# Kernel tuning notes

Hardware: AMD Instinct MI355X
Metric: run time of the kernel (lower is better)

## Reference

```python
import jax, jax.numpy as jnp
import numpy as np

N_NODES = 50000
NUM_FEATS = 512
HIDDEN = 128
NUM_LAYERS = 4
NUM_CLASSES = 40
N_EDGES = 800000
ALPHA = 0.1
C_MIN = 0.2
RESIDUAL_WEIGHT = C_MIN - ALPHA  # 0.1
BIAS_SRELU = -10.0


def setup_inputs() -> dict:
    key = jax.random.key(0)
    ks = jax.random.split(key, 8)
    x = jax.random.normal(ks[0], (N_NODES, NUM_FEATS), dtype=jnp.float32)
    edge_index = jax.random.randint(ks[1], (2, N_EDGES), 0, N_NODES, dtype=jnp.int64)
    W_in = jax.random.normal(ks[2], (NUM_FEATS, HIDDEN), dtype=jnp.float32) / np.sqrt(NUM_FEATS)
    b_in = jnp.zeros((HIDDEN,), dtype=jnp.float32)
    W_layers = jax.random.normal(ks[3], (NUM_LAYERS, HIDDEN, HIDDEN), dtype=jnp.float32) / np.sqrt(HIDDEN)
    srelu_bias = jnp.full((NUM_LAYERS, HIDDEN), BIAS_SRELU, dtype=jnp.float32)
    W_out = jax.random.normal(ks[4], (HIDDEN, NUM_CLASSES), dtype=jnp.float32) / np.sqrt(HIDDEN)
    b_out = jnp.zeros((NUM_CLASSES,), dtype=jnp.float32)
    return {"x": x, "edge_index": edge_index, "W_in": W_in, "b_in": b_in,
            "W_layers": W_layers, "srelu_bias": srelu_bias,
            "W_out": W_out, "b_out": b_out}


def _gcn_norm(edge_index, n):
    # PyG gcn_norm: add self-loops, symmetric normalization D^-1/2 A D^-1/2
    loop = jnp.arange(n, dtype=edge_index.dtype)
    src = jnp.concatenate([edge_index[0], loop])
    dst = jnp.concatenate([edge_index[1], loop])
    ones = jnp.ones(src.shape[0], dtype=jnp.float32)
    deg = jax.ops.segment_sum(ones, dst, num_segments=n)
    dinv = jnp.where(deg > 0, jax.lax.rsqrt(deg), 0.0)
    norm = dinv[src] * dinv[dst]  # [E+N]
    return src, dst, norm


def reference(x, edge_index, W_in, b_in, W_layers, srelu_bias, W_out, b_out):
    n = x.shape[0]
    src, dst, norm = _gcn_norm(edge_index, n)

    # input layer (eval mode: dropout is identity), non-arxiv path
    h = jax.nn.relu(x @ W_in + b_in)
    x0 = h  # original_x residual anchor

    def layer(h, params):
        W, sb = params
        # sparse gather-scale-scatter aggregation: [E, H] messages
        agg = jax.ops.segment_sum(norm[:, None] * h[src], dst, num_segments=n)
        out = (1.0 - ALPHA - RESIDUAL_WEIGHT) * agg + RESIDUAL_WEIGHT * h + ALPHA * x0
        out = out @ W
        out = jax.nn.relu(out - sb) + sb  # SReLU
        return out, None

    h, _ = jax.lax.scan(layer, h, (W_layers, srelu_bias))
    return h @ W_out + b_out
```

## Files before the change

kernel.cpp:

```cpp
#include <hip/hip_runtime.h>
#include <hip/hip_fp16.h>

#define N_NODES 50000
#define E_EDGES 800000
#define F_IN 512
#define HID 128
#define N_LAYERS 4
#define C_OUT 40
#define SCAN_BLOCKS 196

typedef __attribute__((ext_vector_type(8))) short bf16x8;
typedef __attribute__((ext_vector_type(4))) float f32x4;

#define MFMA16(a, b, c) __builtin_amdgcn_mfma_f32_16x16x32_bf16(a, b, c, 0, 0, 0)

__device__ __forceinline__ void split2(float a, unsigned short& hi, unsigned short& lo) {
    unsigned u = __float_as_uint(a);
    unsigned r = u + 0x7FFFu + ((u >> 16) & 1u);
    hi = (unsigned short)(r >> 16);
    float hf = __uint_as_float(((unsigned)hi) << 16);
    lo = (unsigned short)(__float_as_uint(a - hf) >> 16);
}

__device__ __forceinline__ void async16(void* lds, const void* g) {
    __builtin_amdgcn_global_load_lds(
        (const __attribute__((address_space(1))) unsigned*)g,
        (__attribute__((address_space(3))) unsigned*)lds, 16, 0, 0);
}

__global__ void indeg_count(const int* __restrict__ ei, int* __restrict__ indeg) {
    int e = blockIdx.x * 256 + threadIdx.x;
    if (e < E_EDGES) {
        unsigned d = (unsigned)ei[E_EDGES + e];
        if (d < N_NODES) atomicAdd(&indeg[d], 1);
    }
}

__global__ void scan_p1(const int* __restrict__ indeg, int* __restrict__ bsum,
                        float* __restrict__ dinv) {
    __shared__ int red[4];
    int i = blockIdx.x * 256 + threadIdx.x;
    int v = (i < N_NODES) ? indeg[i] : 0;
    if (i < N_NODES) dinv[i] = rsqrtf(1.0f + (float)v);
    int s = v;
    #pragma unroll
    for (int off = 32; off > 0; off >>= 1) s += __shfl_down(s, off, 64);
    if ((threadIdx.x & 63) == 0) red[threadIdx.x >> 6] = s;
    __syncthreads();
    if (threadIdx.x == 0) bsum[blockIdx.x] = red[0] + red[1] + red[2] + red[3];
}

__launch_bounds__(256)
__global__ void scan_p2(const int* __restrict__ bsum, int* __restrict__ boff,
                        int* __restrict__ rowptr) {
    __shared__ int s[256];
    int t = threadIdx.x;
    int v = (t < SCAN_BLOCKS) ? bsum[t] : 0;
    s[t] = v;
    __syncthreads();
    #pragma unroll
    for (int off = 1; off < 256; off <<= 1) {
        int a = s[t];
        int b = (t >= off) ? s[t - off] : 0;
        __syncthreads();
        s[t] = a + b;
        __syncthreads();
    }
    if (t < SCAN_BLOCKS) boff[t] = (t == 0) ? 0 : s[t - 1];
    if (t == 255) rowptr[N_NODES] = s[SCAN_BLOCKS - 1];
}

__launch_bounds__(256)
__global__ void scan_p3(const int* __restrict__ indeg, const int* __restrict__ boff,
                        int* __restrict__ rowptr, int* __restrict__ cursor) {
    __shared__ int s[256];
    int t = threadIdx.x;
    int i = blockIdx.x * 256 + t;
    int v = (i < N_NODES) ? indeg[i] : 0;
    s[t] = v;
    __syncthreads();
    #pragma unroll
    for (int off = 1; off < 256; off <<= 1) {
        int a = s[t];
        int b = (t >= off) ? s[t - off] : 0;
        __syncthreads();
        s[t] = a + b;
        __syncthreads();
    }
    if (i < N_NODES) {
        int excl = boff[blockIdx.x] + s[t] - v;
        rowptr[i] = excl;
        cursor[i] = excl;
    }
}

__global__ void csr_fill(const int* __restrict__ ei, int* __restrict__ cursor,
                         int* __restrict__ csr) {
    int e = blockIdx.x * 256 + threadIdx.x;
    if (e < E_EDGES) {
        unsigned s = (unsigned)ei[e];
        unsigned d = (unsigned)ei[E_EDGES + e];
        if (s < N_NODES && d < N_NODES) {
            int pos = atomicAdd(&cursor[d], 1);
            csr[pos] = (int)s;
        }
    }
}

__global__ void wprep(const float* __restrict__ Wi, const float* __restrict__ Wl,
                      unsigned short* __restrict__ Wth, unsigned short* __restrict__ Wtl,
                      unsigned short* __restrict__ Wlth, unsigned short* __restrict__ Wltl) {
    int idx = blockIdx.x * 256 + threadIdx.x;
    unsigned short hi, lo;
    if (idx < F_IN * HID) {
        int k = idx >> 7, n = idx & 127;
        split2(Wi[idx], hi, lo);
        Wth[(size_t)n * F_IN + k] = hi;
        Wtl[(size_t)n * F_IN + k] = lo;
    } else if (idx < 2 * F_IN * HID) {
        int j = idx - F_IN * HID;
        int l = j >> 14, rem = j & 16383;
        int k = rem >> 7, n = rem & 127;
        split2(Wl[j], hi, lo);
        Wlth[(size_t)l * HID * HID + n * HID + k] = hi;
        Wltl[(size_t)l * HID * HID + n * HID + k] = lo;
    }
}

__launch_bounds__(256)
__global__ void gemm_in_mfma(const float* __restrict__ x,
                             const unsigned short* __restrict__ Bth,
                             const unsigned short* __restrict__ Btl,
                             const float* __restrict__ bi,
                             const float* __restrict__ dinv,
                             float* __restrict__ x0out,
                             __half* __restrict__ g16) {
    __shared__ __align__(16) unsigned short Ah[64 * 32];
    __shared__ __align__(16) unsigned short Al[64 * 32];
    __shared__ __align__(16) unsigned short Bh[128 * 32];
    __shared__ __align__(16) unsigned short Bl[128 * 32];
    const int t = threadIdx.x;
    const int lane = t & 63;
    const int wv = t >> 6;
    const int wr = wv >> 1, wc = wv & 1;
    const int row0 = blockIdx.x * 64;
    const int fr = lane & 15;
    const int fkg = lane >> 4;

    f32x4 acc[2][4] = {};

    for (int step = 0; step < 16; step++) {
        const int k0 = step * 32;
        #pragma unroll
        for (int i = 0; i < 2; i++) {
            int g = t + i * 256;
            int n = g >> 2, kg = g & 3;
            int kgp = kg ^ ((n >> 1) & 3);
            size_t src = (size_t)n * F_IN + k0 + kgp * 8;
            async16(&Bh[g * 8], &Bth[src]);
            async16(&Bl[g * 8], &Btl[src]);
        }
        #pragma unroll
        for (int i = 0; i < 2; i++) {
            int q = t + i * 256;
            int r = q >> 3, c4 = q & 7;
            int grow = row0 + r;
            float4 v = make_float4(0.f, 0.f, 0.f, 0.f);
            if (grow < N_NODES) v = *(const float4*)&x[(size_t)grow * F_IN + k0 + c4 * 4];
            ushort4 uh, ul;
            split2(v.x, uh.x, ul.x); split2(v.y, uh.y, ul.y);
            split2(v.z, uh.z, ul.z); split2(v.w, uh.w, ul.w);
            int gp = (c4 >> 1) ^ ((r >> 1) & 3);
            int idx = r * 32 + gp * 8 + (c4 & 1) * 4;
            *(ushort4*)&Ah[idx] = uh;
            *(ushort4*)&Al[idx] = ul;
        }
        __syncthreads();

        bf16x8 ah[2], al[2];
        #pragma unroll
        for (int mt = 0; mt < 2; mt++) {
            int arow = wr * 32 + mt * 16 + fr;
            int aidx = arow * 32 + (fkg ^ ((arow >> 1) & 3)) * 8;
            ah[mt] = *(bf16x8*)&Ah[aidx];
            al[mt] = *(bf16x8*)&Al[aidx];
        }
        #pragma unroll
        for (int nt = 0; nt < 4; nt++) {
            int n = wc * 64 + nt * 16 + fr;
            int bidx = n * 32 + (fkg ^ ((n >> 1) & 3)) * 8;
            bf16x8 bh = *(bf16x8*)&Bh[bidx];
            bf16x8 bl = *(bf16x8*)&Bl[bidx];
            #pragma unroll
            for (int mt = 0; mt < 2; mt++) {
                acc[mt][nt] = MFMA16(al[mt], bh, acc[mt][nt]);
                acc[mt][nt] = MFMA16(ah[mt], bl, acc[mt][nt]);
                acc[mt][nt] = MFMA16(ah[mt], bh, acc[mt][nt]);
            }
        }
        __syncthreads();
    }

    const int dcol = lane & 15;
    const int dr0 = (lane >> 4) * 4;
    float dv[2][4];
    #pragma unroll
    for (int mt = 0; mt < 2; mt++)
        #pragma unroll
        for (int j = 0; j < 4; j++) {
            int grow = row0 + wr * 32 + mt * 16 + dr0 + j;
            dv[mt][j] = (grow < N_NODES) ? dinv[grow] : 0.f;
        }
    #pragma unroll
    for (int nt = 0; nt < 4; nt++) {
        int gcol = wc * 64 + nt * 16 + dcol;
        float b = bi[gcol];
        #pragma unroll
        for (int mt = 0; mt < 2; mt++) {
            #pragma unroll
            for (int j = 0; j < 4; j++) {
                int grow = row0 + wr * 32 + mt * 16 + dr0 + j;
                if (grow < N_NODES) {
                    float v = fmaxf(acc[mt][nt][j] + b, 0.f);
                    x0out[(size_t)grow * HID + gcol] = v;
                    g16[(size_t)grow * HID + gcol] = __float2half(dv[mt][j] * v);
                }
            }
        }
    }
}

__launch_bounds__(256)
__global__ void aggregate(const int* __restrict__ rowptr, const int* __restrict__ csr,
                          const float* __restrict__ dinv,
                          const __half* __restrict__ g16,
                          const float* __restrict__ h, const float* __restrict__ x0,
                          float* __restrict__ comb) {
    const int node = blockIdx.x * 4 + (threadIdx.x >> 6);
    const int lane = threadIdx.x & 63;
    if (node >= N_NODES) return;

    const unsigned* g32 = (const unsigned*)g16;
    const float dd = dinv[node];
    const int beg = rowptr[node];
    const int end = rowptr[node + 1];

    float a0 = 0.f, a1 = 0.f, b0 = 0.f, b1 = 0.f;

    #define GACC(r, i) { \
        __half2 p = *(__half2*)&(r); \
        float2 f = __half22float2(p); \
        if ((i) & 1) { b0 += f.x; b1 += f.y; } else { a0 += f.x; a1 += f.y; } }

    int e = beg;
    for (; e + 16 <= end; e += 16) {
        unsigned r[16];
        #pragma unroll
        for (int i = 0; i < 16; i++) r[i] = g32[(size_t)csr[e + i] * 64 + lane];
        #pragma unroll
        for (int i = 0; i < 16; i++) GACC(r[i], i)
    }
    for (; e + 4 <= end; e += 4) {
        unsigned r[4];
        #pragma unroll
        for (int i = 0; i < 4; i++) r[i] = g32[(size_t)csr[e + i] * 64 + lane];
        #pragma unroll
        for (int i = 0; i < 4; i++) GACC(r[i], i)
    }
    for (; e < end; e++) {
        unsigned r = g32[(size_t)csr[e] * 64 + lane];
        GACC(r, 0)
    }
    #undef GACC

    float s0 = a0 + b0, s1 = a1 + b1;
    const float c1 = 0.8f * dd;
    const float c2 = 0.8f * dd * dd + 0.1f;
    float2 hv = ((const float2*)h)[(size_t)node * 64 + lane];
    float2 xv = ((const float2*)x0)[(size_t)node * 64 + lane];
    float2 o;
    o.x = fmaf(c1, s0, fmaf(c2, hv.x, 0.1f * xv.x));
    o.y = fmaf(c1, s1, fmaf(c2, hv.y, 0.1f * xv.y));
    ((float2*)comb)[(size_t)node * 64 + lane] = o;
}

__launch_bounds__(256)
__global__ void gemm_layer_mfma(const unsigned short* __restrict__ Bth,
                                const unsigned short* __restrict__ Btl,
                                const float* __restrict__ sb,
                                const float* __restrict__ dinv,
                                float* __restrict__ comb,
                                __half* __restrict__ g16, int writeg) {
    __shared__ __align__(16) unsigned short Ah[64 * 128];
    __shared__ __align__(16) unsigned short Al[64 * 128];
    __shared__ __align__(16) unsigned short Bh[128 * 64];
    __shared__ __align__(16) unsigned short Bl[128 * 64];
    const int t = threadIdx.x;
    const int lane = t & 63;
    const int wv = t >> 6;
    const int wr = wv >> 1, wc = wv & 1;
    const int row0 = blockIdx.x * 64;
    const int fr = lane & 15;
    const int fkg = lane >> 4;

    f32x4 acc[2][4] = {};

    auto stageB = [&](int khalf) {
        #pragma unroll
        for (int i = 0; i < 4; i++) {
            int g = t + i * 256;
            int n = g >> 3, j = g & 7;
            int jp = j ^ (n & 7);
            size_t src = (size_t)n * HID + khalf + jp * 8;
            async16(&Bh[g * 8], &Bth[src]);
            async16(&Bl[g * 8], &Btl[src]);
        }
    };

    stageB(0);
    #pragma unroll
    for (int i = 0; i < 8; i++) {
        int q = t + i * 256;
        int r = q >> 5, c4 = q & 31;
        int grow = row0 + r;
        float4 v = make_float4(0.f, 0.f, 0.f, 0.f);
        if (grow < N_NODES) v = *(const float4*)&comb[(size_t)grow * HID + c4 * 4];
        ushort4 uh, ul;
        split2(v.x, uh.x, ul.x); split2(v.y, uh.y, ul.y);
        split2(v.z, uh.z, ul.z); split2(v.w, uh.w, ul.w);
        int idx = (r * 128 + c4 * 4) ^ ((r & 7) << 3);
        *(ushort4*)&Ah[idx] = uh;
        *(ushort4*)&Al[idx] = ul;
    }
    __syncthreads();

    #pragma unroll
    for (int half = 0; half < 2; half++) {
        #pragma unroll
        for (int kk2 = 0; kk2 < 2; kk2++) {
            int kk = half * 2 + kk2;
            bf16x8 ah[2], al[2];
            #pragma unroll
            for (int mt = 0; mt < 2; mt++) {
                int arow = wr * 32 + mt * 16 + fr;
                int aidx = (arow * 128 + kk * 32 + fkg * 8) ^ ((arow & 7) << 3);
                ah[mt] = *(bf16x8*)&Ah[aidx];
                al[mt] = *(bf16x8*)&Al[aidx];
            }
            #pragma unroll
            for (int nt = 0; nt < 4; nt++) {
                int n = wc * 64 + nt * 16 + fr;
                int bidx = (n * 64 + kk2 * 32 + fkg * 8) ^ ((n & 7) << 3);
                bf16x8 bh = *(bf16x8*)&Bh[bidx];
                bf16x8 bl = *(bf16x8*)&Bl[bidx];
                #pragma unroll
                for (int mt = 0; mt < 2; mt++) {
                    acc[mt][nt] = MFMA16(al[mt], bh, acc[mt][nt]);
                    acc[mt][nt] = MFMA16(ah[mt], bl, acc[mt][nt]);
                    acc[mt][nt] = MFMA16(ah[mt], bh, acc[mt][nt]);
                }
            }
        }
        if (half == 0) {
            __syncthreads();
            stageB(64);
            __syncthreads();
        }
    }

    const int dcol = lane & 15;
    const int dr0 = (lane >> 4) * 4;
    float dv[2][4];
    #pragma unroll
    for (int mt = 0; mt < 2; mt++)
        #pragma unroll
        for (int j = 0; j < 4; j++) {
            int grow = row0 + wr * 32 + mt * 16 + dr0 + j;
            dv[mt][j] = (grow < N_NODES) ? dinv[grow] : 0.f;
        }
    #pragma unroll
    for (int nt = 0; nt < 4; nt++) {
        int gcol = wc * 64 + nt * 16 + dcol;
        float s = sb[gcol];
        #pragma unroll
        for (int mt = 0; mt < 2; mt++) {
            #pragma unroll
            for (int j = 0; j < 4; j++) {
                int grow = row0 + wr * 32 + mt * 16 + dr0 + j;
                if (grow < N_NODES) {
                    float v = fmaxf(acc[mt][nt][j], s);
                    comb[(size_t)grow * HID + gcol] = v;
                    if (writeg) g16[(size_t)grow * HID + gcol] = __float2half(dv[mt][j] * v);
                }
            }
        }
    }
}

__launch_bounds__(256)
__global__ void gemm_out(const float* __restrict__ h, const float* __restrict__ Wo,
                         const float* __restrict__ bo, float* __restrict__ out) {
    __shared__ float As[64][129];
    __shared__ float Ws[128][40];
    const int t = threadIdx.x;
    const int row0 = blockIdx.x * 64;

    #pragma unroll
    for (int i = 0; i < 8; i++) {
        int q = t + i * 256;
        int r = q >> 5, c4 = q & 31;
        int grow = row0 + r;
        float4 v = make_float4(0.f, 0.f, 0.f, 0.f);
        if (grow < N_NODES) v = *(const float4*)&h[(size_t)grow * HID + c4 * 4];
        As[r][c4 * 4 + 0] = v.x;
        As[r][c4 * 4 + 1] = v.y;
        As[r][c4 * 4 + 2] = v.z;
        As[r][c4 * 4 + 3] = v.w;
    }
    #pragma unroll
    for (int i = 0; i < 20; i++) {
        int idx = t + i * 256;
        Ws[idx / 40][idx % 40] = Wo[idx];
    }
    __syncthreads();

    const int r = t >> 2;
    const int c0 = t & 3;
    float acc[10] = {};
    #pragma unroll 4
    for (int k = 0; k < HID; k++) {
        float a = As[r][k];
        #pragma unroll
        for (int i = 0; i < 10; i++) {
            acc[i] = fmaf(a, Ws[k][c0 + 4 * i], acc[i]);
        }
    }
    int grow = row0 + r;
    if (grow < N_NODES) {
        #pragma unroll
        for (int i = 0; i < 10; i++) {
            out[(size_t)grow * C_OUT + c0 + 4 * i] = acc[i] + bo[c0 + 4 * i];
        }
    }
}

extern "C" void kernel_launch(void* const* d_in, const int* in_sizes, int n_in,
                              void* d_out, int out_size, void* d_ws, size_t ws_size,
                              hipStream_t stream) {
    const float* x   = (const float*)d_in[0];
    const int*   ei  = (const int*)d_in[1];
    const float* Wi  = (const float*)d_in[2];
    const float* bi  = (const float*)d_in[3];
    const float* Wls = (const float*)d_in[4];
    const float* sbs = (const float*)d_in[5];
    const float* Wo  = (const float*)d_in[6];
    const float* bo  = (const float*)d_in[7];
    float* out = (float*)d_out;

    float* dinv    = (float*)d_ws;
    int*   indeg   = (int*)(dinv + 50176);
    int*   rowptr  = indeg + 50176;
    int*   cursor  = rowptr + 50304;
    int*   bsum    = cursor + 50176;
    int*   boff    = bsum + 256;
    int*   csr     = boff + 256;
    unsigned short* Wth  = (unsigned short*)(csr + 800000);
    unsigned short* Wtl  = Wth + 65536;
    unsigned short* Wlth = Wtl + 65536;
    unsigned short* Wltl = Wlth + 65536;
    float* x0  = (float*)(Wltl + 65536);
    float* hB  = x0 + (size_t)N_NODES * HID;
    float* hC  = hB + (size_t)N_NODES * HID;
    __half* g16 = (__half*)(hC + (size_t)N_NODES * HID);

    const int edgeBlocks = (E_EDGES + 255) / 256;
    const int gemmBlocks = (N_NODES + 63) / 64;
    const int aggBlocks  = (N_NODES + 3) / 4;

    hipMemsetAsync(indeg, 0, N_NODES * sizeof(int), stream);
    indeg_count<<<edgeBlocks, 256, 0, stream>>>(ei, indeg);
    scan_p1<<<SCAN_BLOCKS, 256, 0, stream>>>(indeg, bsum, dinv);
    scan_p2<<<1, 256, 0, stream>>>(bsum, boff, rowptr);
    scan_p3<<<SCAN_BLOCKS, 256, 0, stream>>>(indeg, boff, rowptr, cursor);
    csr_fill<<<edgeBlocks, 256, 0, stream>>>(ei, cursor, csr);
    wprep<<<(2 * F_IN * HID + 255) / 256, 256, 0, stream>>>(Wi, Wls, Wth, Wtl, Wlth, Wltl);

    gemm_in_mfma<<<gemmBlocks, 256, 0, stream>>>(x, Wth, Wtl, bi, dinv, x0, g16);

    float* h = x0;
    for (int l = 0; l < N_LAYERS; l++) {
        float* next = (l & 1) ? hC : hB;
        aggregate<<<aggBlocks, 256, 0, stream>>>(rowptr, csr, dinv, g16, h, x0, next);
        gemm_layer_mfma<<<gemmBlocks, 256, 0, stream>>>(Wlth + (size_t)l * HID * HID,
                                                        Wltl + (size_t)l * HID * HID,
                                                        sbs + (size_t)l * HID, dinv,
                                                        next, g16,
                                                        (l + 1 < N_LAYERS) ? 1 : 0);
        h = next;
    }

    gemm_out<<<gemmBlocks, 256, 0, stream>>>(h, Wo, bo, out);
}
```

Baseline: 402.6 us.

## Fuse final layer GEMM with output projection and double-buffer input GEMM

```diff
diff --git a/kernel.cpp b/kernel.cpp
--- a/kernel.cpp
+++ b/kernel.cpp
@@ -108,8 +108,10 @@
 }
 
 __global__ void wprep(const float* __restrict__ Wi, const float* __restrict__ Wl,
+                      const float* __restrict__ Wo,
                       unsigned short* __restrict__ Wth, unsigned short* __restrict__ Wtl,
-                      unsigned short* __restrict__ Wlth, unsigned short* __restrict__ Wltl) {
+                      unsigned short* __restrict__ Wlth, unsigned short* __restrict__ Wltl,
+                      unsigned short* __restrict__ Woth, unsigned short* __restrict__ Wotl) {
     int idx = blockIdx.x * 256 + threadIdx.x;
     unsigned short hi, lo;
     if (idx < F_IN * HID) {
@@ -124,6 +126,13 @@
         split2(Wl[j], hi, lo);
         Wlth[(size_t)l * HID * HID + n * HID + k] = hi;
         Wltl[(size_t)l * HID * HID + n * HID + k] = lo;
+    } else if (idx < 2 * F_IN * HID + 48 * HID) {
+        int j = idx - 2 * F_IN * HID;
+        int n = j >> 7, k = j & 127;
+        float w = (n < C_OUT) ? Wo[(size_t)k * C_OUT + n] : 0.f;
+        split2(w, hi, lo);
+        Woth[(size_t)n * HID + k] = hi;
+        Wotl[(size_t)n * HID + k] = lo;
     }
 }
 
@@ -137,8 +146,8 @@
                              __half* __restrict__ g16) {
     __shared__ __align__(16) unsigned short Ah[64 * 32];
     __shared__ __align__(16) unsigned short Al[64 * 32];
-    __shared__ __align__(16) unsigned short Bh[128 * 32];
-    __shared__ __align__(16) unsigned short Bl[128 * 32];
+    __shared__ __align__(16) unsigned short Bh[2][128 * 32];
+    __shared__ __align__(16) unsigned short Bl[2][128 * 32];
     const int t = threadIdx.x;
     const int lane = t & 63;
     const int wv = t >> 6;
@@ -146,41 +155,64 @@
     const int row0 = blockIdx.x * 64;
     const int fr = lane & 15;
     const int fkg = lane >> 4;
+    const float4 z4 = make_float4(0.f, 0.f, 0.f, 0.f);
 
     f32x4 acc[2][4] = {};
 
-    for (int step = 0; step < 16; step++) {
-        const int k0 = step * 32;
+    auto stageB = [&](int buf, int k0) {
         #pragma unroll
         for (int i = 0; i < 2; i++) {
             int g = t + i * 256;
             int n = g >> 2, kg = g & 3;
             int kgp = kg ^ ((n >> 1) & 3);
             size_t src = (size_t)n * F_IN + k0 + kgp * 8;
-            async16(&Bh[g * 8], &Bth[src]);
-            async16(&Bl[g * 8], &Btl[src]);
-        }
+            async16(&Bh[buf][g * 8], &Bth[src]);
+            async16(&Bl[buf][g * 8], &Btl[src]);
+        }
+    };
+    auto loadA = [&](int k0, float4* xr) {
         #pragma unroll
         for (int i = 0; i < 2; i++) {
             int q = t + i * 256;
             int r = q >> 3, c4 = q & 7;
             int grow = row0 + r;
-            float4 v = make_float4(0.f, 0.f, 0.f, 0.f);
-            if (grow < N_NODES) v = *(const float4*)&x[(size_t)grow * F_IN + k0 + c4 * 4];
+            xr[i] = (grow < N_NODES) ? *(const float4*)&x[(size_t)grow * F_IN + k0 + c4 * 4] : z4;
+        }
+    };
+    auto writeA = [&](const float4* xr) {
+        #pragma unroll
+        for (int i = 0; i < 2; i++) {
+            int q = t + i * 256;
+            int r = q >> 3, c4 = q & 7;
             ushort4 uh, ul;
-            split2(v.x, uh.x, ul.x); split2(v.y, uh.y, ul.y);
-            split2(v.z, uh.z, ul.z); split2(v.w, uh.w, ul.w);
+            split2(xr[i].x, uh.x, ul.x); split2(xr[i].y, uh.y, ul.y);
+            split2(xr[i].z, uh.z, ul.z); split2(xr[i].w, uh.w, ul.w);
             int gp = (c4 >> 1) ^ ((r >> 1) & 3);
             int idx = r * 32 + gp * 8 + (c4 & 1) * 4;
             *(ushort4*)&Ah[idx] = uh;
             *(ushort4*)&Al[idx] = ul;
         }
-        __syncthreads();
-
+    };
+
+    float4 xa[2];
+    stageB(0, 0);
+    loadA(0, xa);
+    writeA(xa);
+    __syncthreads();
+
+    int buf = 0;
+    for (int step = 0; step < 16; step++) {
+        float4 xn[2];
+        if (step < 15) {
+            stageB(buf ^ 1, (step + 1) * 32);
+            loadA((step + 1) * 32, xn);
+        }
+
+        int arow0 = wr * 32 + fr;
         bf16x8 ah[2], al[2];
         #pragma unroll
         for (int mt = 0; mt < 2; mt++) {
-            int arow = wr * 32 + mt * 16 + fr;
+            int arow = arow0 + mt * 16;
             int aidx = arow * 32 + (fkg ^ ((arow >> 1) & 3)) * 8;
             ah[mt] = *(bf16x8*)&Ah[aidx];
             al[mt] = *(bf16x8*)&Al[aidx];
@@ -189,8 +221,8 @@
         for (int nt = 0; nt < 4; nt++) {
             int n = wc * 64 + nt * 16 + fr;
             int bidx = n * 32 + (fkg ^ ((n >> 1) & 3)) * 8;
-            bf16x8 bh = *(bf16x8*)&Bh[bidx];
-            bf16x8 bl = *(bf16x8*)&Bl[bidx];
+            bf16x8 bh = *(bf16x8*)&Bh[buf][bidx];
+            bf16x8 bl = *(bf16x8*)&Bl[buf][bidx];
             #pragma unroll
             for (int mt = 0; mt < 2; mt++) {
                 acc[mt][nt] = MFMA16(al[mt], bh, acc[mt][nt]);
@@ -199,6 +231,11 @@
             }
         }
         __syncthreads();
+        if (step < 15) {
+            writeA(xn);
+            buf ^= 1;
+            __syncthreads();
+        }
     }
 
     const int dcol = lane & 15;
@@ -290,11 +327,11 @@
                                 const float* __restrict__ sb,
                                 const float* __restrict__ dinv,
                                 float* __restrict__ comb,
-                                __half* __restrict__ g16, int writeg) {
+                                __half* __restrict__ g16) {
     __shared__ __align__(16) unsigned short Ah[64 * 128];
     __shared__ __align__(16) unsigned short Al[64 * 128];
-    __shared__ __align__(16) unsigned short Bh[128 * 64];
-    __shared__ __align__(16) unsigned short Bl[128 * 64];
+    __shared__ __align__(16) unsigned short Bh[128 * 32];
+    __shared__ __align__(16) unsigned short Bl[128 * 32];
     const int t = threadIdx.x;
     const int lane = t & 63;
     const int wv = t >> 6;
@@ -305,13 +342,13 @@
 
     f32x4 acc[2][4] = {};
 
-    auto stageB = [&](int khalf) {
-        #pragma unroll
-        for (int i = 0; i < 4; i++) {
+    auto stageB = [&](int k0) {
+        #pragma unroll
+        for (int i = 0; i < 2; i++) {
             int g = t + i * 256;
-            int n = g >> 3, j = g & 7;
-            int jp = j ^ (n & 7);
-            size_t src = (size_t)n * HID + khalf + jp * 8;
+            int n = g >> 2, kg = g & 3;
+            int kgp = kg ^ ((n >> 1) & 3);
+            size_t src = (size_t)n * HID + k0 + kgp * 8;
             async16(&Bh[g * 8], &Bth[src]);
             async16(&Bl[g * 8], &Btl[src]);
         }
@@ -335,35 +372,31 @@
     __syncthreads();
 
     #pragma unroll
-    for (int half = 0; half < 2; half++) {
-        #pragma unroll
-        for (int kk2 = 0; kk2 < 2; kk2++) {
-            int kk = half * 2 + kk2;
-            bf16x8 ah[2], al[2];
+    for (int step = 0; step < 4; step++) {
+        bf16x8 ah[2], al[2];
+        #pragma unroll
+        for (int mt = 0; mt < 2; mt++) {
+            int arow = wr * 32 + mt * 16 + fr;
+            int aidx = (arow * 128 + step * 32 + fkg * 8) ^ ((arow & 7) << 3);
+            ah[mt] = *(bf16x8*)&Ah[aidx];
+            al[mt] = *(bf16x8*)&Al[aidx];
+        }
+        #pragma unroll
+        for (int nt = 0; nt < 4; nt++) {
+            int n = wc * 64 + nt * 16 + fr;
+            int bidx = n * 32 + (fkg ^ ((n >> 1) & 3)) * 8;
+            bf16x8 bh = *(bf16x8*)&Bh[bidx];
+            bf16x8 bl = *(bf16x8*)&Bl[bidx];
             #pragma unroll
             for (int mt = 0; mt < 2; mt++) {
-                int arow = wr * 32 + mt * 16 + fr;
-                int aidx = (arow * 128 + kk * 32 + fkg * 8) ^ ((arow & 7) << 3);
-                ah[mt] = *(bf16x8*)&Ah[aidx];
-                al[mt] = *(bf16x8*)&Al[aidx];
+                acc[mt][nt] = MFMA16(al[mt], bh, acc[mt][nt]);
+                acc[mt][nt] = MFMA16(ah[mt], bl, acc[mt][nt]);
+                acc[mt][nt] = MFMA16(ah[mt], bh, acc[mt][nt]);
             }
-            #pragma unroll
-            for (int nt = 0; nt < 4; nt++) {
-                int n = wc * 64 + nt * 16 + fr;
-                int bidx = (n * 64 + kk2 * 32 + fkg * 8) ^ ((n & 7) << 3);
-                bf16x8 bh = *(bf16x8*)&Bh[bidx];
-                bf16x8 bl = *(bf16x8*)&Bl[bidx];
-                #pragma unroll
-                for (int mt = 0; mt < 2; mt++) {
-                    acc[mt][nt] = MFMA16(al[mt], bh, acc[mt][nt]);
-                    acc[mt][nt] = MFMA16(ah[mt], bl, acc[mt][nt]);
-                    acc[mt][nt] = MFMA16(ah[mt], bh, acc[mt][nt]);
-                }
-            }
-        }
-        if (half == 0) {
-            __syncthreads();
-            stageB(64);
+        }
+        __syncthreads();
+        if (step < 3) {
+            stageB((step + 1) * 32);
             __syncthreads();
         }
     }
@@ -390,7 +423,7 @@
                 if (grow < N_NODES) {
                     float v = fmaxf(acc[mt][nt][j], s);
                     comb[(size_t)grow * HID + gcol] = v;
-                    if (writeg) g16[(size_t)grow * HID + gcol] = __float2half(dv[mt][j] * v);
+                    g16[(size_t)grow * HID + gcol] = __float2half(dv[mt][j] * v);
                 }
             }
         }
@@ -398,48 +431,137 @@
 }
 
 __launch_bounds__(256)
-__global__ void gemm_out(const float* __restrict__ h, const float* __restrict__ Wo,
-                         const float* __restrict__ bo, float* __restrict__ out) {
-    __shared__ float As[64][129];
-    __shared__ float Ws[128][40];
+__global__ void gemm_layer_out(const unsigned short* __restrict__ Bth,
+                               const unsigned short* __restrict__ Btl,
+                               const float* __restrict__ sb,
+                               const unsigned short* __restrict__ Woth,
+                               const unsigned short* __restrict__ Wotl,
+                               const float* __restrict__ bo,
+                               const float* __restrict__ comb,
+                               float* __restrict__ out) {
+    __shared__ __align__(16) unsigned short Ah[64 * 128];
+    __shared__ __align__(16) unsigned short Al[64 * 128];
+    __shared__ __align__(16) unsigned short Bh[128 * 32];
+    __shared__ __align__(16) unsigned short Bl[128 * 32];
     const int t = threadIdx.x;
+    const int lane = t & 63;
+    const int wv = t >> 6;
+    const int wr = wv >> 1, wc = wv & 1;
     const int row0 = blockIdx.x * 64;
-
+    const int fr = lane & 15;
+    const int fkg = lane >> 4;
+
+    f32x4 acc[2][4] = {};
+
+    auto stageB = [&](int k0) {
+        #pragma unroll
+        for (int i = 0; i < 2; i++) {
+            int g = t + i * 256;
+            int n = g >> 2, kg = g & 3;
+            int kgp = kg ^ ((n >> 1) & 3);
+            size_t src = (size_t)n * HID + k0 + kgp * 8;
+            async16(&Bh[g * 8], &Bth[src]);
+            async16(&Bl[g * 8], &Btl[src]);
+        }
+    };
+
+    stageB(0);
     #pragma unroll
     for (int i = 0; i < 8; i++) {
         int q = t + i * 256;
         int r = q >> 5, c4 = q & 31;
         int grow = row0 + r;
         float4 v = make_float4(0.f, 0.f, 0.f, 0.f);
-        if (grow < N_NODES) v = *(const float4*)&h[(size_t)grow * HID + c4 * 4];
-        As[r][c4 * 4 + 0] = v.x;
-        As[r][c4 * 4 + 1] = v.y;
-        As[r][c4 * 4 + 2] = v.z;
-        As[r][c4 * 4 + 3] = v.w;
-    }
-    #pragma unroll
-    for (int i = 0; i < 20; i++) {
-        int idx = t + i * 256;
-        Ws[idx / 40][idx % 40] = Wo[idx];
+        if (grow < N_NODES) v = *(const float4*)&comb[(size_t)grow * HID + c4 * 4];
+        ushort4 uh, ul;
+        split2(v.x, uh.x, ul.x); split2(v.y, uh.y, ul.y);
+        split2(v.z, uh.z, ul.z); split2(v.w, uh.w, ul.w);
+        int idx = (r * 128 + c4 * 4) ^ ((r & 7) << 3);
+        *(ushort4*)&Ah[idx] = uh;
+        *(ushort4*)&Al[idx] = ul;
     }
     __syncthreads();
 
-    const int r = t >> 2;
-    const int c0 = t & 3;
-    float acc[10] = {};
-    #pragma unroll 4
-    for (int k = 0; k < HID; k++) {
-        float a = As[r][k];
-        #pragma unroll
-        for (int i = 0; i < 10; i++) {
-            acc[i] = fmaf(a, Ws[k][c0 + 4 * i], acc[i]);
-        }
-    }
-    int grow = row0 + r;
-    if (grow < N_NODES) {
-        #pragma unroll
-        for (int i = 0; i < 10; i++) {
-            out[(size_t)grow * C_OUT + c0 + 4 * i] = acc[i] + bo[c0 + 4 * i];
+    #pragma unroll
+    for (int step = 0; step < 4; step++) {
+        bf16x8 ah[2], al[2];
+        #pragma unroll
+        for (int mt = 0; mt < 2; mt++) {
+            int arow = wr * 32 + mt * 16 + fr;
+            int aidx = (arow * 128 + step * 32 + fkg * 8) ^ ((arow & 7) << 3);
+            ah[mt] = *(bf16x8*)&Ah[aidx];
+            al[mt] = *(bf16x8*)&Al[aidx];
+        }
+        #pragma unroll
+        for (int nt = 0; nt < 4; nt++) {
+            int n = wc * 64 + nt * 16 + fr;
+            int bidx = n * 32 + (fkg ^ ((n >> 1) & 3)) * 8;
+            bf16x8 bh = *(bf16x8*)&Bh[bidx];
+            bf16x8 bl = *(bf16x8*)&Bl[bidx];
+            #pragma unroll
+            for (int mt = 0; mt < 2; mt++) {
+                acc[mt][nt] = MFMA16(al[mt], bh, acc[mt][nt]);
+                acc[mt][nt] = MFMA16(ah[mt], bl, acc[mt][nt]);
+                acc[mt][nt] = MFMA16(ah[mt], bh, acc[mt][nt]);
+            }
+        }
+        __syncthreads();
+        if (step < 3) {
+            stageB((step + 1) * 32);
+            __syncthreads();
+        }
+    }
+
+    const int dcol = lane & 15;
+    const int dr0 = (lane >> 4) * 4;
+    #pragma unroll
+    for (int nt = 0; nt < 4; nt++) {
+        int col = wc * 64 + nt * 16 + dcol;
+        float s = sb[col];
+        #pragma unroll
+        for (int mt = 0; mt < 2; mt++) {
+            #pragma unroll
+            for (int j = 0; j < 4; j++) {
+                int row = wr * 32 + mt * 16 + dr0 + j;
+                float v = fmaxf(acc[mt][nt][j], s);
+                unsigned short hi, lo;
+                split2(v, hi, lo);
+                int idx = (row * 128 + col) ^ ((row & 7) << 3);
+                Ah[idx] = hi;
+                Al[idx] = lo;
+            }
+        }
+    }
+    __syncthreads();
+
+    f32x4 oacc[3] = {};
+    #pragma unroll
+    for (int kk = 0; kk < 4; kk++) {
+        int arow = wv * 16 + fr;
+        int aidx = (arow * 128 + kk * 32 + fkg * 8) ^ ((arow & 7) << 3);
+        bf16x8 ah = *(bf16x8*)&Ah[aidx];
+        bf16x8 al = *(bf16x8*)&Al[aidx];
+        #pragma unroll
+        for (int nt = 0; nt < 3; nt++) {
+            size_t boff = (size_t)(nt * 16 + fr) * HID + kk * 32 + fkg * 8;
+            bf16x8 bh = *(const bf16x8*)&Woth[boff];
+            bf16x8 bl = *(const bf16x8*)&Wotl[boff];
+            oacc[nt] = MFMA16(al, bh, oacc[nt]);
+            oacc[nt] = MFMA16(ah, bl, oacc[nt]);
+            oacc[nt] = MFMA16(ah, bh, oacc[nt]);
+        }
+    }
+    #pragma unroll
+    for (int nt = 0; nt < 3; nt++) {
+        int gcol = nt * 16 + dcol;
+        if (gcol < C_OUT) {
+            float b = bo[gcol];
+            #pragma unroll
+            for (int j = 0; j < 4; j++) {
+                int grow = row0 + wv * 16 + dr0 + j;
+                if (grow < N_NODES)
+                    out[(size_t)grow * C_OUT + gcol] = oacc[nt][j] + b;
+            }
         }
     }
 }
@@ -468,7 +590,9 @@
     unsigned short* Wtl  = Wth + 65536;
     unsigned short* Wlth = Wtl + 65536;
     unsigned short* Wltl = Wlth + 65536;
-    float* x0  = (float*)(Wltl + 65536);
+    unsigned short* Woth = Wltl + 65536;
+    unsigned short* Wotl = Woth + 6144;
+    float* x0  = (float*)(Wotl + 6144);
     float* hB  = x0 + (size_t)N_NODES * HID;
     float* hC  = hB + (size_t)N_NODES * HID;
     __half* g16 = (__half*)(hC + (size_t)N_NODES * HID);
@@ -476,6 +600,7 @@
     const int edgeBlocks = (E_EDGES + 255) / 256;
     const int gemmBlocks = (N_NODES + 63) / 64;
     const int aggBlocks  = (N_NODES + 3) / 4;
+    const int wprepBlocks = (2 * F_IN * HID + 48 * HID + 255) / 256;
 
     hipMemsetAsync(indeg, 0, N_NODES * sizeof(int), stream);
     indeg_count<<<edgeBlocks, 256, 0, stream>>>(ei, indeg);
@@ -483,21 +608,23 @@
     scan_p2<<<1, 256, 0, stream>>>(bsum, boff, rowptr);
     scan_p3<<<SCAN_BLOCKS, 256, 0, stream>>>(indeg, boff, rowptr, cursor);
     csr_fill<<<edgeBlocks, 256, 0, stream>>>(ei, cursor, csr);
-    wprep<<<(2 * F_IN * HID + 255) / 256, 256, 0, stream>>>(Wi, Wls, Wth, Wtl, Wlth, Wltl);
+    wprep<<<wprepBlocks, 256, 0, stream>>>(Wi, Wls, Wo, Wth, Wtl, Wlth, Wltl, Woth, Wotl);
 
     gemm_in_mfma<<<gemmBlocks, 256, 0, stream>>>(x, Wth, Wtl, bi, dinv, x0, g16);
 
     float* h = x0;
-    for (int l = 0; l < N_LAYERS; l++) {
+    for (int l = 0; l < N_LAYERS - 1; l++) {
         float* next = (l & 1) ? hC : hB;
         aggregate<<<aggBlocks, 256, 0, stream>>>(rowptr, csr, dinv, g16, h, x0, next);
         gemm_layer_mfma<<<gemmBlocks, 256, 0, stream>>>(Wlth + (size_t)l * HID * HID,
                                                         Wltl + (size_t)l * HID * HID,
                                                         sbs + (size_t)l * HID, dinv,
-                                                        next, g16,
-                                                        (l + 1 < N_LAYERS) ? 1 : 0);
+                                                        next, g16);
         h = next;
     }
-
-    gemm_out<<<gemmBlocks, 256, 0, stream>>>(h, Wo, bo, out);
-}
+    aggregate<<<aggBlocks, 256, 0, stream>>>(rowptr, csr, dinv, g16, h, x0, hC);
+    gemm_layer_out<<<gemmBlocks, 256, 0, stream>>>(Wlth + (size_t)3 * HID * HID,
+                                                   Wltl + (size_t)3 * HID * HID,
+                                                   sbs + (size_t)3 * HID,
+                                                   Woth, Wotl, bo, hC, out);
+}
```

Result: no change. 405.8 us (+0.8%).
